# Performance work log

Hardware: AMD Instinct MI355X
Metric: run time of the kernel (lower is better)

Reference implementation:

```python
import jax, jax.numpy as jnp
import numpy as np

B, IN, E, H, V, MAX_LEN = 512, 64, 512, 1024, 1024, 32
LN_EPS = 1e-5


def setup_inputs() -> dict:
    key = jax.random.key(0)
    ks = jax.random.split(key, 16)
    s = 0.02
    n = lambda k, shp: jax.random.normal(k, shp, jnp.float32) * s
    return {
        "x": jax.random.normal(ks[0], (B, IN), jnp.float32),
        "w_in": n(ks[1], (E, IN)), "b_in": jnp.zeros((E,), jnp.float32),
        "w_ih0": n(ks[2], (4 * H, E)), "w_hh0": n(ks[3], (4 * H, H)),
        "b_ih0": jnp.zeros((4 * H,), jnp.float32), "b_hh0": jnp.zeros((4 * H,), jnp.float32),
        "w_ih1": n(ks[4], (4 * H, H)), "w_hh1": n(ks[5], (4 * H, H)),
        "b_ih1": jnp.zeros((4 * H,), jnp.float32), "b_hh1": jnp.zeros((4 * H,), jnp.float32),
        "ln_g": jnp.ones((H,), jnp.float32), "ln_b": jnp.zeros((H,), jnp.float32),
        "w_out": n(ks[6], (V, H)), "b_out": jnp.zeros((V,), jnp.float32),
        "emb": n(ks[7], (V, E)),
    }


def _lstm_cell(x, h, c, w_ih, w_hh, b_ih, b_hh):
    # PyTorch LSTMCell: gates ordered (input, forget, cell, output)
    gates = x @ w_ih.T + h @ w_hh.T + b_ih + b_hh  # [B, 4H]
    i, f, g, o = jnp.split(gates, 4, axis=1)
    i, f, o = jax.nn.sigmoid(i), jax.nn.sigmoid(f), jax.nn.sigmoid(o)
    g = jnp.tanh(g)
    c2 = f * c + i * g
    h2 = o * jnp.tanh(c2)
    return h2, c2


def reference(x, w_in, b_in, w_ih0, w_hh0, b_ih0, b_hh0,
              w_ih1, w_hh1, b_ih1, b_hh1, ln_g, ln_b, w_out, b_out, emb):
    bsz = x.shape[0]
    hid = w_hh0.shape[1]
    inp = x @ w_in.T + b_in  # [B, E]
    z = jnp.zeros((bsz, hid), jnp.float32)
    init = (z, z, z, z, inp)

    def step(carry, _):
        h0, c0, h1, c1, cur = carry
        h0, c0 = _lstm_cell(cur, h0, c0, w_ih0, w_hh0, b_ih0, b_hh0)
        h1, c1 = _lstm_cell(h0, h1, c1, w_ih1, w_hh1, b_ih1, b_hh1)
        mu = jnp.mean(h1, axis=-1, keepdims=True)
        var = jnp.mean((h1 - mu) ** 2, axis=-1, keepdims=True)
        hn = (h1 - mu) / jnp.sqrt(var + LN_EPS) * ln_g + ln_b
        lp = jax.nn.log_softmax(hn @ w_out.T + b_out, axis=-1)  # [B, V]
        ent = -jnp.sum(jnp.exp(lp) * lp, axis=-1)  # [B]
        sym = jnp.argmax(lp, axis=-1)  # eval-mode (deterministic) path
        logprob = jnp.take_along_axis(lp, sym[:, None], axis=1)[:, 0]
        nxt = emb[sym]  # [B, E]
        return (h0, c0, h1, c1, nxt), (sym, logprob, ent)

    _, (seq, logits, ent) = jax.lax.scan(step, init, None, length=MAX_LEN)
    seq, logits, ent = seq.T, logits.T, ent.T  # [B, MAX_LEN]
    zcol_f = jnp.zeros((bsz, 1), jnp.float32)
    zcol_i = jnp.zeros((bsz, 1), seq.dtype)
    seq = jnp.concatenate([seq, zcol_i], axis=1)
    logits = jnp.concatenate([logits, zcol_f], axis=1)
    ent = jnp.concatenate([ent, zcol_f], axis=1)
    return seq, logits, ent
```

## Files before the change

kernel.cpp:

```cpp
#include <hip/hip_runtime.h>
#include <hip/hip_bf16.h>
#include <math.h>

#define BQ   512
#define EDIM 512
#define HDIM 1024
#define VDIM 1024
#define TLEN 32
#define TOUT 33
#define PGS  (BQ * 4 * HDIM)
#define PLS  (BQ * VDIM)

typedef _Float16 half8  __attribute__((ext_vector_type(8)));
typedef _Float16 half4v __attribute__((ext_vector_type(4)));
typedef float    f32x16 __attribute__((ext_vector_type(16)));

#define GLOAD_LDS16(gp, lp) __builtin_amdgcn_global_load_lds( \
    (const __attribute__((address_space(1))) void*)(gp),      \
    (__attribute__((address_space(3))) void*)(lp), 16, 0, 0)

__device__ __forceinline__ size_t packoff(int r, int k, int K) {
    return (size_t)(r >> 5) * (size_t)(32 * K) + (size_t)(k >> 4) * 512
         + (size_t)((k >> 3) & 1) * 256 + (size_t)(r & 31) * 8 + (size_t)(k & 7);
}

__device__ _Float16 g_curh[BQ*EDIM], g_curl[BQ*EDIM];
__device__ _Float16 g_h0h[BQ*HDIM], g_h0l[BQ*HDIM];
__device__ _Float16 g_h1h[BQ*HDIM], g_h1l[BQ*HDIM];
__device__ _Float16 g_hnh[BQ*HDIM], g_hnl[BQ*HDIM];
__device__ float    g_c0[BQ*HDIM], g_c1[BQ*HDIM];

__device__ _Float16 g_wih0h[4*HDIM*EDIM], g_wih0l[4*HDIM*EDIM];
__device__ _Float16 g_whh0h[4*HDIM*HDIM], g_whh0l[4*HDIM*HDIM];
__device__ _Float16 g_wih1h[4*HDIM*HDIM], g_wih1l[4*HDIM*HDIM];
__device__ _Float16 g_whh1h[4*HDIM*HDIM], g_whh1l[4*HDIM*HDIM];
__device__ _Float16 g_wouth[VDIM*HDIM],   g_woutl[VDIM*HDIM];

__device__ float g_part_g[2 * PGS];
__device__ float g_part_lg[8 * PLS];
__device__ float g_bsum0[4*HDIM], g_bsum1[4*HDIM];

__global__ void init_kernel(float* __restrict__ out,
                            const float* __restrict__ bi0, const float* __restrict__ bh0,
                            const float* __restrict__ bi1, const float* __restrict__ bh1) {
    int i = blockIdx.x * 256 + threadIdx.x;
    g_c0[i] = 0.f; g_c1[i] = 0.f;
    g_h0h[i] = (_Float16)0.f; g_h0l[i] = (_Float16)0.f;
    g_h1h[i] = (_Float16)0.f; g_h1l[i] = (_Float16)0.f;
    if (i < 4 * HDIM) {
        g_bsum0[i] = bi0[i] + bh0[i];
        g_bsum1[i] = bi1[i] + bh1[i];
    }
    if (i < 3 * BQ) {
        int which = i / BQ, b = i % BQ;
        out[(size_t)which * BQ * TOUT + (size_t)b * TOUT + (TOUT - 1)] = 0.f;
    }
}

__global__ void split_pack_kernel(const float* __restrict__ w, _Float16* __restrict__ hi,
                                  _Float16* __restrict__ lo, int klog, int nquads) {
    int q = blockIdx.x * 256 + threadIdx.x;
    if (q >= nquads) return;
    int e = q * 4;
    int r = e >> klog, k = e & ((1 << klog) - 1);
    float4 v = ((const float4*)w)[q];
    half4v h, l;
    h[0] = (_Float16)v.x; l[0] = (_Float16)((v.x - (float)h[0]) * 4096.f);
    h[1] = (_Float16)v.y; l[1] = (_Float16)((v.y - (float)h[1]) * 4096.f);
    h[2] = (_Float16)v.z; l[2] = (_Float16)((v.z - (float)h[2]) * 4096.f);
    h[3] = (_Float16)v.w; l[3] = (_Float16)((v.w - (float)h[3]) * 4096.f);
    size_t po = packoff(r, k, 1 << klog);
    *(half4v*)&hi[po] = h;
    *(half4v*)&lo[po] = l;
}

__device__ __forceinline__ void split1(float x, _Float16* hp, _Float16* lp) {
    _Float16 h = (_Float16)x;
    *hp = h;
    *lp = (_Float16)((x - (float)h) * 4096.f);
}

__global__ __launch_bounds__(512, 2) void gemm_big(
    const _Float16* __restrict__ Ah1, const _Float16* __restrict__ Al1, int K1,
    const _Float16* __restrict__ Wh1, const _Float16* __restrict__ Wl1,
    const _Float16* __restrict__ Ah2, const _Float16* __restrict__ Al2, int K2,
    const _Float16* __restrict__ Wh2, const _Float16* __restrict__ Wl2,
    const float* __restrict__ bias, float* __restrict__ outp,
    int N, int S, int NTP)
{
    __shared__ __align__(16) _Float16 sA[4][2][4][2][512];
    __shared__ __align__(16) _Float16 sB[4][2][4][2][512];
    int tid = threadIdx.x;
    int l = tid & 63, w = tid >> 6;
    int lr = l & 31, lq = l >> 5;
    int mw = w >> 2, nw = w & 3;

    int wb = blockIdx.x;
    int xcd = wb & 7, q = wb >> 3;
    int nt = xcd * NTP + q % NTP;
    int rest = q / NTP;
    int s = rest % S;
    int mb = rest / S;

    int kch1 = K1 / S, kch2 = (K2 > 0) ? (K2 / S) : 0;
    int n1 = kch1 >> 5;
    int nit = n1 + (kch2 >> 5);

    const _Float16* fsrc1[4];
    const _Float16* fsrc2[4];
    _Float16* fdst0[4];
    #pragma unroll
    for (int qq = 0; qq < 4; ++qq) {
        int fq = w * 4 + qq;
        bool isA = fq < 16;
        int r_ = isA ? fq : fq - 16;
        int pl = r_ >> 3, idx = (r_ >> 1) & 3, kh = r_ & 1;
        int strip = isA ? (mb * 4 + idx) : (nt * 4 + idx);
        const _Float16* p1 = isA ? (pl ? Al1 : Ah1) : (pl ? Wl1 : Wh1);
        fsrc1[qq] = p1 + (size_t)strip * (size_t)(32 * K1)
                  + (size_t)((s * kch1) >> 4) * 512 + (size_t)kh * 512 + (size_t)l * 8;
        if (K2 > 0) {
            const _Float16* p2 = isA ? (pl ? Al2 : Ah2) : (pl ? Wl2 : Wh2);
            fsrc2[qq] = p2 + (size_t)strip * (size_t)(32 * K2)
                      + (size_t)((s * kch2) >> 4) * 512 + (size_t)kh * 512 + (size_t)l * 8;
        } else {
            fsrc2[qq] = fsrc1[qq];
        }
        fdst0[qq] = isA ? &sA[0][pl][idx][kh][0] : &sB[0][pl][idx][kh][0];
    }

    f32x16 accM0 = {}, accM1 = {}, accL0 = {}, accL1 = {};

#define STAGE(IT, SLOT)                                                        \
    {                                                                          \
        int it_ = (IT);                                                        \
        bool g1_ = it_ < n1;                                                   \
        size_t off_ = (size_t)(g1_ ? it_ : it_ - n1) * 1024;                   \
        _Pragma("unroll")                                                      \
        for (int qq = 0; qq < 4; ++qq) {                                       \
            const _Float16* sp_ = (g1_ ? fsrc1[qq] : fsrc2[qq]) + off_;        \
            GLOAD_LDS16(sp_, fdst0[qq] + (size_t)(SLOT) * 8192);               \
        }                                                                      \
    }

#define COMPUTE(BUF)                                                           \
    {                                                                          \
        _Pragma("unroll")                                                      \
        for (int kh_ = 0; kh_ < 2; ++kh_) {                                    \
            half8 ah0 = *(const half8*)&sA[BUF][0][2*mw  ][kh_][(size_t)l * 8];\
            half8 ah1 = *(const half8*)&sA[BUF][0][2*mw+1][kh_][(size_t)l * 8];\
            half8 al0 = *(const half8*)&sA[BUF][1][2*mw  ][kh_][(size_t)l * 8];\
            half8 al1 = *(const half8*)&sA[BUF][1][2*mw+1][kh_][(size_t)l * 8];\
            half8 bh  = *(const half8*)&sB[BUF][0][nw][kh_][(size_t)l * 8];    \
            half8 bl  = *(const half8*)&sB[BUF][1][nw][kh_][(size_t)l * 8];    \
            accM0 = __builtin_amdgcn_mfma_f32_32x32x16_f16(ah0, bh, accM0, 0, 0, 0); \
            accM1 = __builtin_amdgcn_mfma_f32_32x32x16_f16(ah1, bh, accM1, 0, 0, 0); \
            accL0 = __builtin_amdgcn_mfma_f32_32x32x16_f16(ah0, bl, accL0, 0, 0, 0); \
            accL1 = __builtin_amdgcn_mfma_f32_32x32x16_f16(ah1, bl, accL1, 0, 0, 0); \
            accL0 = __builtin_amdgcn_mfma_f32_32x32x16_f16(al0, bh, accL0, 0, 0, 0); \
            accL1 = __builtin_amdgcn_mfma_f32_32x32x16_f16(al1, bh, accL1, 0, 0, 0); \
        }                                                                      \
    }

#define WAITSYNC(IT)                                                           \
    {                                                                          \
        if ((IT) < nit - 2)       asm volatile("s_waitcnt vmcnt(8)" ::: "memory"); \
        else if ((IT) == nit - 2) asm volatile("s_waitcnt vmcnt(4)" ::: "memory"); \
        else                      asm volatile("s_waitcnt vmcnt(0)" ::: "memory"); \
        __builtin_amdgcn_sched_barrier(0);                                     \
        __builtin_amdgcn_s_barrier();                                          \
    }

#define ITER(IT, BUF)                                                          \
    {                                                                          \
        if ((IT) + 2 < nit) STAGE((IT) + 2, ((BUF) + 2) & 3);                  \
        WAITSYNC(IT);                                                          \
        COMPUTE(BUF);                                                          \
    }

    STAGE(0, 0);
    STAGE(1, 1);
    for (int base = 0; base < nit; base += 4) {
        ITER(base + 0, 0);
        ITER(base + 1, 1);
        ITER(base + 2, 2);
        ITER(base + 3, 3);
    }
#undef ITER
#undef WAITSYNC
#undef COMPUTE
#undef STAGE

    int n = nt * 128 + nw * 32 + lr;
    int m0 = mb * 128 + mw * 64;
    float bv = bias ? bias[n] : 0.f;
    float* op = outp + (size_t)s * BQ * N;
    #pragma unroll
    for (int r = 0; r < 16; ++r) {
        int row = (r & 3) + 8 * (r >> 2) + 4 * lq;
        op[(size_t)(m0 + row) * N + n]      = accM0[r] + accL0[r] * (1.f / 4096.f) + bv;
        op[(size_t)(m0 + 32 + row) * N + n] = accM1[r] + accL1[r] * (1.f / 4096.f) + bv;
    }
}

#define GBK 16
#define GPAD 68
__global__ __launch_bounds__(256) void gemm_in(const float* __restrict__ x,
                                               const float* __restrict__ w_in,
                                               const float* __restrict__ b_in) {
    __shared__ __align__(16) float As[GBK][GPAD];
    __shared__ __align__(16) float Bs[GBK][GPAD];
    int tid = threadIdx.x;
    int tx = tid & 15, ty = tid >> 4;
    int m0 = blockIdx.y * 64, n0 = blockIdx.x * 64;
    int lm = tid >> 2, lk = (tid & 3) << 2;
    const int K = 64;
    float acc[4][4] = {};
    for (int k0 = 0; k0 < K; k0 += GBK) {
        float4 av = *(const float4*)(x + (size_t)(m0 + lm) * K + k0 + lk);
        float4 wv = *(const float4*)(w_in + (size_t)(n0 + lm) * K + k0 + lk);
        As[lk + 0][lm] = av.x; As[lk + 1][lm] = av.y;
        As[lk + 2][lm] = av.z; As[lk + 3][lm] = av.w;
        Bs[lk + 0][lm] = wv.x; Bs[lk + 1][lm] = wv.y;
        Bs[lk + 2][lm] = wv.z; Bs[lk + 3][lm] = wv.w;
        __syncthreads();
        #pragma unroll
        for (int kk = 0; kk < GBK; ++kk) {
            float4 a  = *(const float4*)&As[kk][ty * 4];
            float4 bq = *(const float4*)&Bs[kk][tx * 4];
            float aa[4] = {a.x, a.y, a.z, a.w};
            float bb[4] = {bq.x, bq.y, bq.z, bq.w};
            #pragma unroll
            for (int i = 0; i < 4; ++i)
                #pragma unroll
                for (int j = 0; j < 4; ++j)
                    acc[i][j] = fmaf(aa[i], bb[j], acc[i][j]);
        }
        __syncthreads();
    }
    #pragma unroll
    for (int i = 0; i < 4; ++i) {
        int m = m0 + ty * 4 + i;
        int n = n0 + tx * 4;
        half4v h, lo;
        #pragma unroll
        for (int j = 0; j < 4; ++j) {
            float v = acc[i][j] + b_in[n + j];
            _Float16 hv = (_Float16)v;
            h[j] = hv;
            lo[j] = (_Float16)((v - (float)hv) * 4096.f);
        }
        size_t po = packoff(m, n, EDIM);
        *(half4v*)&g_curh[po] = h;
        *(half4v*)&g_curl[po] = lo;
    }
}

__device__ __forceinline__ float sigm(float x) { return 1.f / (1.f + expf(-x)); }

__global__ void lstm0_kernel() {
    int qidx = blockIdx.x * 256 + threadIdx.x;
    int b = qidx >> 8;
    int j = (qidx & 255) * 4;
    size_t base = (size_t)b * 4096;
    float4 G[4];
    #pragma unroll
    for (int g = 0; g < 4; ++g) {
        float4 p0 = *(const float4*)&g_part_g[base + g * 1024 + j];
        float4 p1 = *(const float4*)&g_part_g[PGS + base + g * 1024 + j];
        float4 bs = *(const float4*)&g_bsum0[g * 1024 + j];
        G[g].x = p0.x + p1.x + bs.x;
        G[g].y = p0.y + p1.y + bs.y;
        G[g].z = p0.z + p1.z + bs.z;
        G[g].w = p0.w + p1.w + bs.w;
    }
    size_t hb = (size_t)b * HDIM + j;
    float4 cin = *(const float4*)&g_c0[hb];
    float ci[4] = {cin.x, cin.y, cin.z, cin.w};
    float gi[4] = {G[0].x, G[0].y, G[0].z, G[0].w};
    float gf[4] = {G[1].x, G[1].y, G[1].z, G[1].w};
    float gg[4] = {G[2].x, G[2].y, G[2].z, G[2].w};
    float go[4] = {G[3].x, G[3].y, G[3].z, G[3].w};
    float c[4], h[4];
    half4v hh, hl;
    #pragma unroll
    for (int r = 0; r < 4; ++r) {
        c[r] = sigm(gf[r]) * ci[r] + sigm(gi[r]) * tanhf(gg[r]);
        h[r] = sigm(go[r]) * tanhf(c[r]);
        _Float16 hi16 = (_Float16)h[r];
        hh[r] = hi16;
        hl[r] = (_Float16)((h[r] - (float)hi16) * 4096.f);
    }
    *(float4*)&g_c0[hb] = {c[0], c[1], c[2], c[3]};
    size_t po = packoff(b, j, HDIM);
    *(half4v*)&g_h0h[po] = hh;
    *(half4v*)&g_h0l[po] = hl;
}

__global__ __launch_bounds__(256) void lstm1_ln_kernel(
    const float* __restrict__ ln_g, const float* __restrict__ ln_b)
{
    __shared__ float sbuf[4];
    int b = blockIdx.x, tid = threadIdx.x;
    int lane = tid & 63, wid = tid >> 6;
    int j = tid * 4;
    size_t base = (size_t)b * 4096;
    float4 G[4];
    #pragma unroll
    for (int g = 0; g < 4; ++g) {
        float4 p0 = *(const float4*)&g_part_g[base + g * 1024 + j];
        float4 p1 = *(const float4*)&g_part_g[PGS + base + g * 1024 + j];
        float4 bs = *(const float4*)&g_bsum1[g * 1024 + j];
        G[g].x = p0.x + p1.x + bs.x;
        G[g].y = p0.y + p1.y + bs.y;
        G[g].z = p0.z + p1.z + bs.z;
        G[g].w = p0.w + p1.w + bs.w;
    }
    size_t hb = (size_t)b * HDIM + j;
    float4 cin = *(const float4*)&g_c1[hb];
    float ci[4] = {cin.x, cin.y, cin.z, cin.w};
    float gi[4] = {G[0].x, G[0].y, G[0].z, G[0].w};
    float gf[4] = {G[1].x, G[1].y, G[1].z, G[1].w};
    float gg[4] = {G[2].x, G[2].y, G[2].z, G[2].w};
    float go[4] = {G[3].x, G[3].y, G[3].z, G[3].w};
    float c[4], h[4];
    float sum = 0.f;
    #pragma unroll
    for (int r = 0; r < 4; ++r) {
        c[r] = sigm(gf[r]) * ci[r] + sigm(gi[r]) * tanhf(gg[r]);
        h[r] = sigm(go[r]) * tanhf(c[r]);
        sum += h[r];
    }
    *(float4*)&g_c1[hb] = {c[0], c[1], c[2], c[3]};
    size_t po = packoff(b, j, HDIM);
    half4v h1h, h1l;
    #pragma unroll
    for (int r = 0; r < 4; ++r) {
        _Float16 hi16 = (_Float16)h[r];
        h1h[r] = hi16;
        h1l[r] = (_Float16)((h[r] - (float)hi16) * 4096.f);
    }
    *(half4v*)&g_h1h[po] = h1h;
    *(half4v*)&g_h1l[po] = h1l;

    for (int off = 32; off > 0; off >>= 1) sum += __shfl_down(sum, off, 64);
    if (lane == 0) sbuf[wid] = sum;
    __syncthreads();
    float mu = (sbuf[0] + sbuf[1] + sbuf[2] + sbuf[3]) * (1.f / HDIM);
    __syncthreads();
    float sq = 0.f;
    #pragma unroll
    for (int r = 0; r < 4; ++r) { float d = h[r] - mu; sq += d * d; }
    for (int off = 32; off > 0; off >>= 1) sq += __shfl_down(sq, off, 64);
    if (lane == 0) sbuf[wid] = sq;
    __syncthreads();
    float var = (sbuf[0] + sbuf[1] + sbuf[2] + sbuf[3]) * (1.f / HDIM);
    float rstd = 1.f / sqrtf(var + 1e-5f);
    half4v nh, nl;
    #pragma unroll
    for (int r = 0; r < 4; ++r) {
        float hn = (h[r] - mu) * rstd * ln_g[j + r] + ln_b[j + r];
        _Float16 hi16 = (_Float16)hn;
        nh[r] = hi16;
        nl[r] = (_Float16)((hn - (float)hi16) * 4096.f);
    }
    *(half4v*)&g_hnh[po] = nh;
    *(half4v*)&g_hnl[po] = nl;
}

__global__ __launch_bounds__(256) void softmax_row_kernel(
    const float* __restrict__ b_out, const float* __restrict__ emb,
    float* __restrict__ out, int t)
{
    __shared__ float swv[4];
    __shared__ int   swi[4];
    __shared__ float sZ[4], sS[4];
    __shared__ float s_max;
    __shared__ int   s_idx;
    int b = blockIdx.x, tid = threadIdx.x;
    int lane = tid & 63, wid = tid >> 6;
    size_t base = (size_t)b * VDIM + 4 * tid;
    float4 xv = *(const float4*)&b_out[4 * tid];
    #pragma unroll
    for (int s = 0; s < 8; ++s) {
        float4 p = *(const float4*)&g_part_lg[(size_t)s * PLS + base];
        xv.x += p.x; xv.y += p.y; xv.z += p.z; xv.w += p.w;
    }

    float mv = xv.x; int mi = 4 * tid;
    if (xv.y > mv) { mv = xv.y; mi = 4 * tid + 1; }
    if (xv.z > mv) { mv = xv.z; mi = 4 * tid + 2; }
    if (xv.w > mv) { mv = xv.w; mi = 4 * tid + 3; }
    for (int off = 32; off > 0; off >>= 1) {
        float ov = __shfl_down(mv, off, 64);
        int   oi = __shfl_down(mi, off, 64);
        if (ov > mv || (ov == mv && oi < mi)) { mv = ov; mi = oi; }
    }
    if (lane == 0) { swv[wid] = mv; swi[wid] = mi; }
    __syncthreads();
    if (tid == 0) {
        mv = swv[0]; mi = swi[0];
        for (int w = 1; w < 4; ++w)
            if (swv[w] > mv || (swv[w] == mv && swi[w] < mi)) { mv = swv[w]; mi = swi[w]; }
        s_max = mv; s_idx = mi;
    }
    __syncthreads();
    float xmax = s_max;

    float sv[4] = {xv.x - xmax, xv.y - xmax, xv.z - xmax, xv.w - xmax};
    float z = 0.f, s1 = 0.f;
    #pragma unroll
    for (int r = 0; r < 4; ++r) { float e = expf(sv[r]); z += e; s1 += e * sv[r]; }
    for (int off = 32; off > 0; off >>= 1) {
        z  += __shfl_down(z, off, 64);
        s1 += __shfl_down(s1, off, 64);
    }
    if (lane == 0) { sZ[wid] = z; sS[wid] = s1; }
    __syncthreads();
    if (tid == 0) {
        float Z = sZ[0] + sZ[1] + sZ[2] + sZ[3];
        float S1 = sS[0] + sS[1] + sS[2] + sS[3];
        float logZ = logf(Z);
        float ent = logZ - S1 / Z;
        out[(size_t)b * TOUT + t]                         = (float)s_idx;
        out[(size_t)BQ * TOUT + (size_t)b * TOUT + t]     = -logZ;
        out[(size_t)2 * BQ * TOUT + (size_t)b * TOUT + t] = ent;
    }
    __syncthreads();
    int sym = s_idx;
    const float* e = emb + (size_t)sym * EDIM;
    for (int j = tid; j < EDIM; j += 256) {
        size_t po = packoff(b, j, EDIM);
        split1(e[j], &g_curh[po], &g_curl[po]);
    }
}

extern "C" void kernel_launch(void* const* d_in, const int* in_sizes, int n_in,
                              void* d_out, int out_size, void* d_ws, size_t ws_size,
                              hipStream_t stream) {
    const float* x     = (const float*)d_in[0];
    const float* w_in  = (const float*)d_in[1];
    const float* b_in  = (const float*)d_in[2];
    const float* w_ih0 = (const float*)d_in[3];
    const float* w_hh0 = (const float*)d_in[4];
    const float* b_ih0 = (const float*)d_in[5];
    const float* b_hh0 = (const float*)d_in[6];
    const float* w_ih1 = (const float*)d_in[7];
    const float* w_hh1 = (const float*)d_in[8];
    const float* b_ih1 = (const float*)d_in[9];
    const float* b_hh1 = (const float*)d_in[10];
    const float* ln_g  = (const float*)d_in[11];
    const float* ln_b  = (const float*)d_in[12];
    const float* w_out = (const float*)d_in[13];
    const float* b_out = (const float*)d_in[14];
    const float* emb   = (const float*)d_in[15];
    float* out = (float*)d_out;

    _Float16 *wih0h, *wih0l, *whh0h, *whh0l, *wih1h, *wih1l, *whh1h, *whh1l, *wouth, *woutl;
    hipGetSymbolAddress((void**)&wih0h, HIP_SYMBOL(g_wih0h));
    hipGetSymbolAddress((void**)&wih0l, HIP_SYMBOL(g_wih0l));
    hipGetSymbolAddress((void**)&whh0h, HIP_SYMBOL(g_whh0h));
    hipGetSymbolAddress((void**)&whh0l, HIP_SYMBOL(g_whh0l));
    hipGetSymbolAddress((void**)&wih1h, HIP_SYMBOL(g_wih1h));
    hipGetSymbolAddress((void**)&wih1l, HIP_SYMBOL(g_wih1l));
    hipGetSymbolAddress((void**)&whh1h, HIP_SYMBOL(g_whh1h));
    hipGetSymbolAddress((void**)&whh1l, HIP_SYMBOL(g_whh1l));
    hipGetSymbolAddress((void**)&wouth, HIP_SYMBOL(g_wouth));
    hipGetSymbolAddress((void**)&woutl, HIP_SYMBOL(g_woutl));
    _Float16 *curh, *curl, *h0h, *h0l, *h1h, *h1l, *hnh, *hnl;
    hipGetSymbolAddress((void**)&curh, HIP_SYMBOL(g_curh));
    hipGetSymbolAddress((void**)&curl, HIP_SYMBOL(g_curl));
    hipGetSymbolAddress((void**)&h0h, HIP_SYMBOL(g_h0h));
    hipGetSymbolAddress((void**)&h0l, HIP_SYMBOL(g_h0l));
    hipGetSymbolAddress((void**)&h1h, HIP_SYMBOL(g_h1h));
    hipGetSymbolAddress((void**)&h1l, HIP_SYMBOL(g_h1l));
    hipGetSymbolAddress((void**)&hnh, HIP_SYMBOL(g_hnh));
    hipGetSymbolAddress((void**)&hnl, HIP_SYMBOL(g_hnl));
    float *part_g, *part_lg;
    hipGetSymbolAddress((void**)&part_g, HIP_SYMBOL(g_part_g));
    hipGetSymbolAddress((void**)&part_lg, HIP_SYMBOL(g_part_lg));

    init_kernel<<<(BQ * HDIM) / 256, 256, 0, stream>>>(out, b_ih0, b_hh0, b_ih1, b_hh1);

    split_pack_kernel<<<(4*HDIM*EDIM/4 + 255)/256, 256, 0, stream>>>(w_ih0, wih0h, wih0l, 9,  4*HDIM*EDIM/4);
    split_pack_kernel<<<(4*HDIM*HDIM/4 + 255)/256, 256, 0, stream>>>(w_hh0, whh0h, whh0l, 10, 4*HDIM*HDIM/4);
    split_pack_kernel<<<(4*HDIM*HDIM/4 + 255)/256, 256, 0, stream>>>(w_ih1, wih1h, wih1l, 10, 4*HDIM*HDIM/4);
    split_pack_kernel<<<(4*HDIM*HDIM/4 + 255)/256, 256, 0, stream>>>(w_hh1, whh1h, whh1l, 10, 4*HDIM*HDIM/4);
    split_pack_kernel<<<(VDIM*HDIM/4 + 255)/256, 256, 0, stream>>>(w_out, wouth, woutl, 10, VDIM*HDIM/4);

    gemm_in<<<dim3(EDIM / 64, BQ / 64), 256, 0, stream>>>(x, w_in, b_in);

    for (int t = 0; t < TLEN; ++t) {
        gemm_big<<<256, 512, 0, stream>>>(
            curh, curl, EDIM, wih0h, wih0l,
            h0h, h0l, HDIM, whh0h, whh0l,
            (const float*)nullptr, part_g, 4 * HDIM, 2, 4);
        lstm0_kernel<<<(BQ * HDIM / 4) / 256, 256, 0, stream>>>();

        gemm_big<<<256, 512, 0, stream>>>(
            h0h, h0l, HDIM, wih1h, wih1l,
            h1h, h1l, HDIM, whh1h, whh1l,
            (const float*)nullptr, part_g, 4 * HDIM, 2, 4);
        lstm1_ln_kernel<<<BQ, 256, 0, stream>>>(ln_g, ln_b);

        gemm_big<<<256, 512, 0, stream>>>(
            hnh, hnl, HDIM, wouth, woutl,
            (const _Float16*)nullptr, (const _Float16*)nullptr, 0,
            (const _Float16*)nullptr, (const _Float16*)nullptr,
            (const float*)nullptr, part_lg, VDIM, 8, 1);

        softmax_row_kernel<<<BQ, 256, 0, stream>>>(b_out, emb, out, t);
    }
}
```

Measured before the change: 2.842 ms.

## Register-block GEMM with 4 waves each computing a 64x64 tile

The split-fp16 GEMM is restructured from 8 waves each owning a 64x32 output tile to 4 waves each owning a 64x64 tile. Each wave now keeps eight MFMA accumulators and reuses every A and B fragment it loads from LDS twice, which cuts LDS reads per MFMA. The K step per stage is halved to 16, so the pipeline has twice as many iterations with smaller LDS buffers. The trade-off is more accumulator registers per wave and fewer waves per block to hide latency. The unused bias parameter is also removed.

```diff
diff --git a/kernel.cpp b/kernel.cpp
--- a/kernel.cpp
+++ b/kernel.cpp
@@ -80,20 +80,19 @@
     *lp = (_Float16)((x - (float)h) * 4096.f);
 }
 
-__global__ __launch_bounds__(512, 2) void gemm_big(
+__global__ __launch_bounds__(256, 2) void gemm_rb(
     const _Float16* __restrict__ Ah1, const _Float16* __restrict__ Al1, int K1,
     const _Float16* __restrict__ Wh1, const _Float16* __restrict__ Wl1,
     const _Float16* __restrict__ Ah2, const _Float16* __restrict__ Al2, int K2,
     const _Float16* __restrict__ Wh2, const _Float16* __restrict__ Wl2,
-    const float* __restrict__ bias, float* __restrict__ outp,
-    int N, int S, int NTP)
+    float* __restrict__ outp, int N, int S, int NTP)
 {
-    __shared__ __align__(16) _Float16 sA[4][2][4][2][512];
-    __shared__ __align__(16) _Float16 sB[4][2][4][2][512];
+    __shared__ __align__(16) _Float16 sA[4][2][4][512];
+    __shared__ __align__(16) _Float16 sB[4][2][4][512];
     int tid = threadIdx.x;
     int l = tid & 63, w = tid >> 6;
     int lr = l & 31, lq = l >> 5;
-    int mw = w >> 2, nw = w & 3;
+    int mw = w >> 1, nw = w & 1;
 
     int wb = blockIdx.x;
     int xcd = wb & 7, q = wb >> 3;
@@ -103,8 +102,8 @@
     int mb = rest / S;
 
     int kch1 = K1 / S, kch2 = (K2 > 0) ? (K2 / S) : 0;
-    int n1 = kch1 >> 5;
-    int nit = n1 + (kch2 >> 5);
+    int n1 = kch1 >> 4;
+    int nit = n1 + (kch2 >> 4);
 
     const _Float16* fsrc1[4];
     const _Float16* fsrc2[4];
@@ -112,54 +111,60 @@
     #pragma unroll
     for (int qq = 0; qq < 4; ++qq) {
         int fq = w * 4 + qq;
-        bool isA = fq < 16;
-        int r_ = isA ? fq : fq - 16;
-        int pl = r_ >> 3, idx = (r_ >> 1) & 3, kh = r_ & 1;
+        bool isA = fq < 8;
+        int r_ = isA ? fq : fq - 8;
+        int pl = r_ >> 2, idx = r_ & 3;
         int strip = isA ? (mb * 4 + idx) : (nt * 4 + idx);
         const _Float16* p1 = isA ? (pl ? Al1 : Ah1) : (pl ? Wl1 : Wh1);
         fsrc1[qq] = p1 + (size_t)strip * (size_t)(32 * K1)
-                  + (size_t)((s * kch1) >> 4) * 512 + (size_t)kh * 512 + (size_t)l * 8;
+                  + (size_t)((s * kch1) >> 4) * 512 + (size_t)l * 8;
         if (K2 > 0) {
             const _Float16* p2 = isA ? (pl ? Al2 : Ah2) : (pl ? Wl2 : Wh2);
             fsrc2[qq] = p2 + (size_t)strip * (size_t)(32 * K2)
-                      + (size_t)((s * kch2) >> 4) * 512 + (size_t)kh * 512 + (size_t)l * 8;
+                      + (size_t)((s * kch2) >> 4) * 512 + (size_t)l * 8;
         } else {
             fsrc2[qq] = fsrc1[qq];
         }
-        fdst0[qq] = isA ? &sA[0][pl][idx][kh][0] : &sB[0][pl][idx][kh][0];
-    }
-
-    f32x16 accM0 = {}, accM1 = {}, accL0 = {}, accL1 = {};
+        fdst0[qq] = isA ? &sA[0][pl][idx][0] : &sB[0][pl][idx][0];
+    }
+
+    f32x16 accM00 = {}, accM01 = {}, accM10 = {}, accM11 = {};
+    f32x16 accL00 = {}, accL01 = {}, accL10 = {}, accL11 = {};
 
 #define STAGE(IT, SLOT)                                                        \
     {                                                                          \
         int it_ = (IT);                                                        \
         bool g1_ = it_ < n1;                                                   \
-        size_t off_ = (size_t)(g1_ ? it_ : it_ - n1) * 1024;                   \
+        size_t off_ = (size_t)(g1_ ? it_ : it_ - n1) * 512;                    \
         _Pragma("unroll")                                                      \
         for (int qq = 0; qq < 4; ++qq) {                                       \
             const _Float16* sp_ = (g1_ ? fsrc1[qq] : fsrc2[qq]) + off_;        \
-            GLOAD_LDS16(sp_, fdst0[qq] + (size_t)(SLOT) * 8192);               \
+            GLOAD_LDS16(sp_, fdst0[qq] + (size_t)(SLOT) * 4096);               \
         }                                                                      \
     }
 
 #define COMPUTE(BUF)                                                           \
     {                                                                          \
-        _Pragma("unroll")                                                      \
-        for (int kh_ = 0; kh_ < 2; ++kh_) {                                    \
-            half8 ah0 = *(const half8*)&sA[BUF][0][2*mw  ][kh_][(size_t)l * 8];\
-            half8 ah1 = *(const half8*)&sA[BUF][0][2*mw+1][kh_][(size_t)l * 8];\
-            half8 al0 = *(const half8*)&sA[BUF][1][2*mw  ][kh_][(size_t)l * 8];\
-            half8 al1 = *(const half8*)&sA[BUF][1][2*mw+1][kh_][(size_t)l * 8];\
-            half8 bh  = *(const half8*)&sB[BUF][0][nw][kh_][(size_t)l * 8];    \
-            half8 bl  = *(const half8*)&sB[BUF][1][nw][kh_][(size_t)l * 8];    \
-            accM0 = __builtin_amdgcn_mfma_f32_32x32x16_f16(ah0, bh, accM0, 0, 0, 0); \
-            accM1 = __builtin_amdgcn_mfma_f32_32x32x16_f16(ah1, bh, accM1, 0, 0, 0); \
-            accL0 = __builtin_amdgcn_mfma_f32_32x32x16_f16(ah0, bl, accL0, 0, 0, 0); \
-            accL1 = __builtin_amdgcn_mfma_f32_32x32x16_f16(ah1, bl, accL1, 0, 0, 0); \
-            accL0 = __builtin_amdgcn_mfma_f32_32x32x16_f16(al0, bh, accL0, 0, 0, 0); \
-            accL1 = __builtin_amdgcn_mfma_f32_32x32x16_f16(al1, bh, accL1, 0, 0, 0); \
-        }                                                                      \
+        half8 ah0 = *(const half8*)&sA[BUF][0][2*mw  ][(size_t)l * 8];         \
+        half8 ah1 = *(const half8*)&sA[BUF][0][2*mw+1][(size_t)l * 8];         \
+        half8 al0 = *(const half8*)&sA[BUF][1][2*mw  ][(size_t)l * 8];         \
+        half8 al1 = *(const half8*)&sA[BUF][1][2*mw+1][(size_t)l * 8];         \
+        half8 bh0 = *(const half8*)&sB[BUF][0][2*nw  ][(size_t)l * 8];         \
+        half8 bh1 = *(const half8*)&sB[BUF][0][2*nw+1][(size_t)l * 8];         \
+        half8 bl0 = *(const half8*)&sB[BUF][1][2*nw  ][(size_t)l * 8];         \
+        half8 bl1 = *(const half8*)&sB[BUF][1][2*nw+1][(size_t)l * 8];         \
+        accM00 = __builtin_amdgcn_mfma_f32_32x32x16_f16(ah0, bh0, accM00, 0, 0, 0); \
+        accM01 = __builtin_amdgcn_mfma_f32_32x32x16_f16(ah0, bh1, accM01, 0, 0, 0); \
+        accM10 = __builtin_amdgcn_mfma_f32_32x32x16_f16(ah1, bh0, accM10, 0, 0, 0); \
+        accM11 = __builtin_amdgcn_mfma_f32_32x32x16_f16(ah1, bh1, accM11, 0, 0, 0); \
+        accL00 = __builtin_amdgcn_mfma_f32_32x32x16_f16(ah0, bl0, accL00, 0, 0, 0); \
+        accL01 = __builtin_amdgcn_mfma_f32_32x32x16_f16(ah0, bl1, accL01, 0, 0, 0); \
+        accL10 = __builtin_amdgcn_mfma_f32_32x32x16_f16(ah1, bl0, accL10, 0, 0, 0); \
+        accL11 = __builtin_amdgcn_mfma_f32_32x32x16_f16(ah1, bl1, accL11, 0, 0, 0); \
+        accL00 = __builtin_amdgcn_mfma_f32_32x32x16_f16(al0, bh0, accL00, 0, 0, 0); \
+        accL01 = __builtin_amdgcn_mfma_f32_32x32x16_f16(al0, bh1, accL01, 0, 0, 0); \
+        accL10 = __builtin_amdgcn_mfma_f32_32x32x16_f16(al1, bh0, accL10, 0, 0, 0); \
+        accL11 = __builtin_amdgcn_mfma_f32_32x32x16_f16(al1, bh1, accL11, 0, 0, 0); \
     }
 
 #define WAITSYNC(IT)                                                           \
@@ -171,35 +176,34 @@
         __builtin_amdgcn_s_barrier();                                          \
     }
 
-#define ITER(IT, BUF)                                                          \
-    {                                                                          \
-        if ((IT) + 2 < nit) STAGE((IT) + 2, ((BUF) + 2) & 3);                  \
-        WAITSYNC(IT);                                                          \
-        COMPUTE(BUF);                                                          \
-    }
-
     STAGE(0, 0);
     STAGE(1, 1);
-    for (int base = 0; base < nit; base += 4) {
-        ITER(base + 0, 0);
-        ITER(base + 1, 1);
-        ITER(base + 2, 2);
-        ITER(base + 3, 3);
-    }
-#undef ITER
+    for (int it = 0; it < nit; ++it) {
+        if (it + 2 < nit) STAGE(it + 2, (it + 2) & 3);
+        WAITSYNC(it);
+        COMPUTE(it & 3);
+    }
 #undef WAITSYNC
 #undef COMPUTE
 #undef STAGE
 
-    int n = nt * 128 + nw * 32 + lr;
-    int m0 = mb * 128 + mw * 64;
-    float bv = bias ? bias[n] : 0.f;
     float* op = outp + (size_t)s * BQ * N;
     #pragma unroll
-    for (int r = 0; r < 16; ++r) {
-        int row = (r & 3) + 8 * (r >> 2) + 4 * lq;
-        op[(size_t)(m0 + row) * N + n]      = accM0[r] + accL0[r] * (1.f / 4096.f) + bv;
-        op[(size_t)(m0 + 32 + row) * N + n] = accM1[r] + accL1[r] * (1.f / 4096.f) + bv;
+    for (int mi = 0; mi < 2; ++mi) {
+        int m0 = mb * 128 + (mw * 2 + mi) * 32;
+        #pragma unroll
+        for (int ni = 0; ni < 2; ++ni) {
+            int n = nt * 128 + (nw * 2 + ni) * 32 + lr;
+            const f32x16* aM = (mi == 0) ? (ni == 0 ? &accM00 : &accM01)
+                                         : (ni == 0 ? &accM10 : &accM11);
+            const f32x16* aL = (mi == 0) ? (ni == 0 ? &accL00 : &accL01)
+                                         : (ni == 0 ? &accL10 : &accL11);
+            #pragma unroll
+            for (int r = 0; r < 16; ++r) {
+                int row = (r & 3) + 8 * (r >> 2) + 4 * lq;
+                op[(size_t)(m0 + row) * N + n] = (*aM)[r] + (*aL)[r] * (1.f / 4096.f);
+            }
+        }
     }
 }
 
@@ -491,23 +495,23 @@
     gemm_in<<<dim3(EDIM / 64, BQ / 64), 256, 0, stream>>>(x, w_in, b_in);
 
     for (int t = 0; t < TLEN; ++t) {
-        gemm_big<<<256, 512, 0, stream>>>(
+        gemm_rb<<<256, 256, 0, stream>>>(
             curh, curl, EDIM, wih0h, wih0l,
             h0h, h0l, HDIM, whh0h, whh0l,
-            (const float*)nullptr, part_g, 4 * HDIM, 2, 4);
+            part_g, 4 * HDIM, 2, 4);
         lstm0_kernel<<<(BQ * HDIM / 4) / 256, 256, 0, stream>>>();
 
-        gemm_big<<<256, 512, 0, stream>>>(
+        gemm_rb<<<256, 256, 0, stream>>>(
             h0h, h0l, HDIM, wih1h, wih1l,
             h1h, h1l, HDIM, whh1h, whh1l,
-            (const float*)nullptr, part_g, 4 * HDIM, 2, 4);
+            part_g, 4 * HDIM, 2, 4);
         lstm1_ln_kernel<<<BQ, 256, 0, stream>>>(ln_g, ln_b);
 
-        gemm_big<<<256, 512, 0, stream>>>(
+        gemm_rb<<<256, 256, 0, stream>>>(
             hnh, hnl, HDIM, wouth, woutl,
             (const _Float16*)nullptr, (const _Float16*)nullptr, 0,
             (const _Float16*)nullptr, (const _Float16*)nullptr,
-            (const float*)nullptr, part_lg, VDIM, 8, 1);
+            part_lg, VDIM, 8, 1);
 
         softmax_row_kernel<<<BQ, 256, 0, stream>>>(b_out, emb, out, t);
     }
```

Measured after the change: 3.005 ms. 1.06x slower.
